# Kernel tuning notes

Hardware: AMD Instinct MI355X
Metric: run time of the kernel (lower is better)

Reference implementation:

```python
import math
import jax, jax.numpy as jnp
import numpy as np

N, T, F, H = 30000, 4, 128, 8  # num_node, num_type, num_fea, num_head
D = F // H


def setup_inputs() -> dict:
    key = jax.random.key(0)
    k0, k1, k2, k3, k4 = jax.random.split(key, 5)
    feature = jax.random.normal(k0, (N, F), dtype=jnp.float32)
    edge_fea = jax.random.normal(k1, (N, T, F), dtype=jnp.float32)
    node_multi_mask = jax.random.randint(k2, (N,), 0, T)
    # Xavier-uniform-like scale for [*, F, F] projection tables
    xav = math.sqrt(6.0 / (F + F))
    node_proj = jax.random.uniform(k3, (T, F, F), minval=-xav, maxval=xav, dtype=jnp.float32)
    edge_proj = jax.random.uniform(k4, (T * T, F, F), minval=-xav, maxval=xav, dtype=jnp.float32)
    return {
        "feature": feature,
        "edge_fea": edge_fea,
        "node_multi_mask": node_multi_mask,
        "node_proj": node_proj,
        "edge_proj": edge_proj,
    }


def reference(feature, edge_fea, node_multi_mask, node_proj, edge_proj):
    # Type-indexed projections. Instead of gathering per-node [F,F] matrices
    # (which would materialize N*F*F), compute projections for all T source
    # types in one batched einsum, then select each node's type with a gather.
    # node: out[n] = node_proj[mask[n]] @ feature[n]
    node_all = jnp.einsum('tgf,nf->ntg', node_proj, feature)           # [N,T,F]
    node_p = jnp.take_along_axis(node_all, node_multi_mask[:, None, None], axis=1)[:, 0]  # [N,F]
    # edge: out[n,j] = edge_proj[mask[n]*T + j] @ edge_fea[n,j]
    edge_proj_r = edge_proj.reshape(T, T, F, F)                         # [src_type, j, F, F]
    edge_all = jnp.einsum('stgf,ntf->nstg', edge_proj_r, edge_fea)      # [N,T_src,T,F]
    edge_p = jnp.take_along_axis(edge_all, node_multi_mask[:, None, None, None], axis=1)[:, 0]  # [N,T,F]

    # multi-head attention weights
    node_multi_in = node_p.reshape(N, 1, H, D).transpose(0, 2, 1, 3) / math.sqrt(D)  # [N,H,1,D]
    edge_multi_in = edge_p.reshape(N, T, H, D).transpose(0, 2, 3, 1)                  # [N,H,D,T]
    scores = jnp.matmul(node_multi_in, edge_multi_in)                                 # [N,H,1,T]
    # NOTE: original uses nn.Softmax(dim=1) -> softmax over the HEAD axis
    all_r_weight = jax.nn.softmax(scores, axis=1).transpose(0, 3, 1, 2)               # [N,T,H,1]
    return all_r_weight
```

## Files before the change

### kernel.cpp

```cpp
#include <hip/hip_runtime.h>
#include <hip/hip_bf16.h>

#define N_NODES 30000
#define T_TYPES 4
#define F_DIM   128
#define H_HEADS 8

typedef __bf16 bf16x8 __attribute__((ext_vector_type(8)));
typedef __bf16 bf16x4 __attribute__((ext_vector_type(4)));
typedef float  floatx4 __attribute__((ext_vector_type(4)));

#define WS_REORDER 64
#define WS_NPB     480256
#define WS_EPB     611328

template <int CTRL>
static __device__ __forceinline__ float dpp_add(float x) {
    int xi = __builtin_bit_cast(int, x);
    int yi = __builtin_amdgcn_update_dpp(xi, xi, CTRL, 0xF, 0xF, true);
    return x + __builtin_bit_cast(float, yi);
}
static __device__ __forceinline__ float sum16(float x) {
    x = dpp_add<0xB1>(x);
    x = dpp_add<0x4E>(x);
    x = dpp_add<0x141>(x);
    x = dpp_add<0x140>(x);
    return x;
}

__global__ __launch_bounds__(256) void prep_bucket_kernel(
    const float* __restrict__ node_proj, const float* __restrict__ edge_proj,
    __bf16* __restrict__ npb, __bf16* __restrict__ epb,
    const int* __restrict__ mask, int* __restrict__ counts, int* __restrict__ reorder)
{
    const int b = blockIdx.x;
    if (b < 320) {
        int i = b * 256 + threadIdx.x;
        int base = i * 4;
        float4 v;
        __bf16* dst;
        if (base < T_TYPES * F_DIM * F_DIM) {
            v = ((const float4*)node_proj)[i];
            dst = npb + base;
        } else {
            int off = base - T_TYPES * F_DIM * F_DIM;
            v = ((const float4*)edge_proj)[off >> 2];
            dst = epb + off;
        }
        bf16x4 w = { (__bf16)v.x, (__bf16)v.y, (__bf16)v.z, (__bf16)v.w };
        *(bf16x4*)dst = w;
    } else {
        int n = (b - 320) * 256 + threadIdx.x;
        int lane = threadIdx.x & 63;
        int t = (n < N_NODES) ? mask[n] : -1;
        #pragma unroll
        for (int tt = 0; tt < T_TYPES; ++tt) {
            unsigned long long bm = __ballot(t == tt);
            if (bm == 0ull) continue;
            int cnt = __popcll(bm);
            int leader = __ffsll((unsigned long long)bm) - 1;
            int base = 0;
            if (lane == leader) base = atomicAdd(&counts[tt], cnt);
            base = __shfl(base, leader);
            if (t == tt) {
                int prefix = __popcll(bm & ((1ull << lane) - 1ull));
                reorder[tt * N_NODES + base + prefix] = n;
            }
        }
    }
}

__global__ __launch_bounds__(512) void main_kernel(
    const float* __restrict__ feature, const float* __restrict__ edge_fea,
    const int* __restrict__ counts, const int* __restrict__ reorder,
    const __bf16* __restrict__ npb, const __bf16* __restrict__ epb,
    float* __restrict__ out)
{
    const int b = blockIdx.x;
    const int t = b & 3;
    const int start = (b >> 2) * 32;
    const int Nt = counts[t];
    if (start >= Nt) return;
    const int valid = min(32, Nt - start);

    __shared__ __bf16 Afeat[32][136];
    __shared__ __bf16 Aedge[4][32][136];
    __shared__ float  sc[32][4][H_HEADS + 1];
    __shared__ int    nidx[32];

    const int tid = threadIdx.x;
    if (tid < 32) {
        int s = (tid < valid) ? tid : (valid - 1);
        nidx[tid] = reorder[t * N_NODES + start + s];
    }
    __syncthreads();

    const int colv = tid & 31;
    const int rowg = tid >> 5;
    #pragma unroll
    for (int it = 0; it < 2; ++it) {
        int row = it * 16 + rowg;
        float4 v = ((const float4*)(feature + (long)nidx[row] * F_DIM))[colv];
        bf16x4 w = { (__bf16)v.x, (__bf16)v.y, (__bf16)v.z, (__bf16)v.w };
        *(bf16x4*)(&Afeat[row][0] + colv * 4) = w;
    }
    #pragma unroll
    for (int it = 0; it < 8; ++it) {
        int row = it * 16 + rowg;
        int j = row >> 5, r = row & 31;
        float4 v = ((const float4*)(edge_fea + ((long)nidx[r] * 4 + j) * F_DIM))[colv];
        bf16x4 w = { (__bf16)v.x, (__bf16)v.y, (__bf16)v.z, (__bf16)v.w };
        *(bf16x4*)(&Aedge[j][r][0] + colv * 4) = w;
    }
    __syncthreads();

    const int lane = tid & 63;
    const int wave = tid >> 6;
    const int ml   = lane & 15;
    const int quad = lane >> 4;
    const int g0   = wave * 16;

    floatx4 accN[2] = {};
    {
        const __bf16* a0 = &Afeat[ml][quad * 8];
        const __bf16* a1 = &Afeat[16 + ml][quad * 8];
        const __bf16* b0 = npb + t * (F_DIM * F_DIM) + (g0 + ml) * F_DIM + quad * 8;
        #pragma unroll
        for (int k0 = 0; k0 < 128; k0 += 32) {
            bf16x8 A0 = *(const bf16x8*)(a0 + k0);
            bf16x8 A1 = *(const bf16x8*)(a1 + k0);
            bf16x8 B0 = *(const bf16x8*)(b0 + k0);
            accN[0] = __builtin_amdgcn_mfma_f32_16x16x32_bf16(A0, B0, accN[0], 0, 0, 0);
            accN[1] = __builtin_amdgcn_mfma_f32_16x16x32_bf16(A1, B0, accN[1], 0, 0, 0);
        }
    }

    #pragma unroll
    for (int j = 0; j < 4; ++j) {
        floatx4 accE[2] = {};
        const __bf16* a0 = &Aedge[j][ml][quad * 8];
        const __bf16* a1 = &Aedge[j][16 + ml][quad * 8];
        const __bf16* b0 = epb + (t * 4 + j) * (F_DIM * F_DIM) + (g0 + ml) * F_DIM + quad * 8;
        #pragma unroll
        for (int k0 = 0; k0 < 128; k0 += 32) {
            bf16x8 A0 = *(const bf16x8*)(a0 + k0);
            bf16x8 A1 = *(const bf16x8*)(a1 + k0);
            bf16x8 B0 = *(const bf16x8*)(b0 + k0);
            accE[0] = __builtin_amdgcn_mfma_f32_16x16x32_bf16(A0, B0, accE[0], 0, 0, 0);
            accE[1] = __builtin_amdgcn_mfma_f32_16x16x32_bf16(A1, B0, accE[1], 0, 0, 0);
        }
        #pragma unroll
        for (int mt = 0; mt < 2; ++mt) {
            floatx4 p = accN[mt] * accE[mt];
            p.x = sum16(p.x);
            p.y = sum16(p.y);
            p.z = sum16(p.z);
            p.w = sum16(p.w);
            if (ml == 0) {
                int mb = mt * 16 + quad * 4;
                sc[mb + 0][j][wave] = p.x * 0.25f;
                sc[mb + 1][j][wave] = p.y * 0.25f;
                sc[mb + 2][j][wave] = p.z * 0.25f;
                sc[mb + 3][j][wave] = p.w * 0.25f;
            }
        }
    }
    __syncthreads();

    if (tid < 128) {
        int node = tid >> 2, j = tid & 3;
        if (node < valid) {
            float v[8], m = -1e30f;
            #pragma unroll
            for (int h = 0; h < 8; ++h) { v[h] = sc[node][j][h]; m = fmaxf(m, v[h]); }
            float s = 0.f;
            #pragma unroll
            for (int h = 0; h < 8; ++h) { v[h] = __expf(v[h] - m); s += v[h]; }
            float r = 1.0f / s;
            float* o = out + (long)nidx[node] * (T_TYPES * H_HEADS) + j * H_HEADS;
            float4 o0 = { v[0] * r, v[1] * r, v[2] * r, v[3] * r };
            float4 o1 = { v[4] * r, v[5] * r, v[6] * r, v[7] * r };
            ((float4*)o)[0] = o0;
            ((float4*)o)[1] = o1;
        }
    }
}

extern "C" void kernel_launch(void* const* d_in, const int* in_sizes, int n_in,
                              void* d_out, int out_size, void* d_ws, size_t ws_size,
                              hipStream_t stream) {
    const float* feature   = (const float*)d_in[0];
    const float* edge_fea  = (const float*)d_in[1];
    const int*   mask      = (const int*)d_in[2];
    const float* node_proj = (const float*)d_in[3];
    const float* edge_proj = (const float*)d_in[4];
    float* out = (float*)d_out;

    char* ws = (char*)d_ws;
    int*    counts  = (int*)ws;
    int*    reorder = (int*)(ws + WS_REORDER);
    __bf16* npb     = (__bf16*)(ws + WS_NPB);
    __bf16* epb     = (__bf16*)(ws + WS_EPB);

    hipMemsetAsync(counts, 0, T_TYPES * sizeof(int), stream);
    int prep_blocks = 320;
    int bucket_blocks = (N_NODES + 255) / 256;
    prep_bucket_kernel<<<prep_blocks + bucket_blocks, 256, 0, stream>>>(
        node_proj, edge_proj, npb, epb, mask, counts, reorder);
    int nblk = ((N_NODES + 31) / 32) * T_TYPES;
    main_kernel<<<nblk, 512, 0, stream>>>(feature, edge_fea, counts, reorder, npb, epb, out);
}
```

Before: 145.2 us.

## Compact block grid by type prefix sums and prefetch projection weights into registers

The main kernel now maps blocks to node types through prefix sums of the per-type counts, so the grid shrinks from four times the node-block count to about one times that, with no early-exit blocks. The node and first edge projection B fragments are loaded from global memory before the barrier, overlapping with the staging of the activation tiles. The next edge type's weights are prefetched during the current type's MFMAs, with a scheduling barrier to keep that order. An occupancy hint is added to the launch bounds. The cost is higher register pressure from holding the prefetched weight fragments.

```diff
diff --git a/kernel.cpp b/kernel.cpp
--- a/kernel.cpp
+++ b/kernel.cpp
@@ -70,17 +70,21 @@
     }
 }
 
-__global__ __launch_bounds__(512) void main_kernel(
+__global__ __launch_bounds__(512, 6) void main_kernel(
     const float* __restrict__ feature, const float* __restrict__ edge_fea,
     const int* __restrict__ counts, const int* __restrict__ reorder,
     const __bf16* __restrict__ npb, const __bf16* __restrict__ epb,
     float* __restrict__ out)
 {
     const int b = blockIdx.x;
-    const int t = b & 3;
-    const int start = (b >> 2) * 32;
-    const int Nt = counts[t];
-    if (start >= Nt) return;
+    const int c0 = counts[0], c1 = counts[1], c2 = counts[2], c3 = counts[3];
+    const int nb0 = (c0 + 31) >> 5, nb1 = (c1 + 31) >> 5, nb2 = (c2 + 31) >> 5, nb3 = (c3 + 31) >> 5;
+    const int p1 = nb0, p2 = p1 + nb1, p3 = p2 + nb2, p4 = p3 + nb3;
+    if (b >= p4) return;
+    const int t = (b >= p1) + (b >= p2) + (b >= p3);
+    const int pb = (t == 0) ? 0 : (t == 1) ? p1 : (t == 2) ? p2 : p3;
+    const int Nt = (t == 0) ? c0 : (t == 1) ? c1 : (t == 2) ? c2 : c3;
+    const int start = (b - pb) * 32;
     const int valid = min(32, Nt - start);
 
     __shared__ __bf16 Afeat[32][136];
@@ -94,6 +98,12 @@
         nidx[tid] = reorder[t * N_NODES + start + s];
     }
     __syncthreads();
+
+    const int lane = tid & 63;
+    const int wave = tid >> 6;
+    const int ml   = lane & 15;
+    const int quad = lane >> 4;
+    const int g0   = wave * 16;
 
     const int colv = tid & 31;
     const int rowg = tid >> 5;
@@ -112,58 +122,98 @@
         bf16x4 w = { (__bf16)v.x, (__bf16)v.y, (__bf16)v.z, (__bf16)v.w };
         *(bf16x4*)(&Aedge[j][r][0] + colv * 4) = w;
     }
+
+    const __bf16* bn  = npb + t * (F_DIM * F_DIM) + (g0 + ml) * F_DIM + quad * 8;
+    const __bf16* be  = epb + (t * 4) * (F_DIM * F_DIM) + (g0 + ml) * F_DIM + quad * 8;
+    bf16x8 Bn0 = *(const bf16x8*)(bn +  0);
+    bf16x8 Bn1 = *(const bf16x8*)(bn + 32);
+    bf16x8 Bn2 = *(const bf16x8*)(bn + 64);
+    bf16x8 Bn3 = *(const bf16x8*)(bn + 96);
+    bf16x8 Bc0 = *(const bf16x8*)(be +  0);
+    bf16x8 Bc1 = *(const bf16x8*)(be + 32);
+    bf16x8 Bc2 = *(const bf16x8*)(be + 64);
+    bf16x8 Bc3 = *(const bf16x8*)(be + 96);
     __syncthreads();
 
-    const int lane = tid & 63;
-    const int wave = tid >> 6;
-    const int ml   = lane & 15;
-    const int quad = lane >> 4;
-    const int g0   = wave * 16;
-
-    floatx4 accN[2] = {};
+    floatx4 accN0 = {0.f, 0.f, 0.f, 0.f};
+    floatx4 accN1 = {0.f, 0.f, 0.f, 0.f};
     {
         const __bf16* a0 = &Afeat[ml][quad * 8];
         const __bf16* a1 = &Afeat[16 + ml][quad * 8];
-        const __bf16* b0 = npb + t * (F_DIM * F_DIM) + (g0 + ml) * F_DIM + quad * 8;
-        #pragma unroll
-        for (int k0 = 0; k0 < 128; k0 += 32) {
-            bf16x8 A0 = *(const bf16x8*)(a0 + k0);
-            bf16x8 A1 = *(const bf16x8*)(a1 + k0);
-            bf16x8 B0 = *(const bf16x8*)(b0 + k0);
-            accN[0] = __builtin_amdgcn_mfma_f32_16x16x32_bf16(A0, B0, accN[0], 0, 0, 0);
-            accN[1] = __builtin_amdgcn_mfma_f32_16x16x32_bf16(A1, B0, accN[1], 0, 0, 0);
-        }
+        bf16x8 A00 = *(const bf16x8*)(a0 +  0);
+        bf16x8 A10 = *(const bf16x8*)(a1 +  0);
+        bf16x8 A01 = *(const bf16x8*)(a0 + 32);
+        bf16x8 A11 = *(const bf16x8*)(a1 + 32);
+        bf16x8 A02 = *(const bf16x8*)(a0 + 64);
+        bf16x8 A12 = *(const bf16x8*)(a1 + 64);
+        bf16x8 A03 = *(const bf16x8*)(a0 + 96);
+        bf16x8 A13 = *(const bf16x8*)(a1 + 96);
+        accN0 = __builtin_amdgcn_mfma_f32_16x16x32_bf16(A00, Bn0, accN0, 0, 0, 0);
+        accN1 = __builtin_amdgcn_mfma_f32_16x16x32_bf16(A10, Bn0, accN1, 0, 0, 0);
+        accN0 = __builtin_amdgcn_mfma_f32_16x16x32_bf16(A01, Bn1, accN0, 0, 0, 0);
+        accN1 = __builtin_amdgcn_mfma_f32_16x16x32_bf16(A11, Bn1, accN1, 0, 0, 0);
+        accN0 = __builtin_amdgcn_mfma_f32_16x16x32_bf16(A02, Bn2, accN0, 0, 0, 0);
+        accN1 = __builtin_amdgcn_mfma_f32_16x16x32_bf16(A12, Bn2, accN1, 0, 0, 0);
+        accN0 = __builtin_amdgcn_mfma_f32_16x16x32_bf16(A03, Bn3, accN0, 0, 0, 0);
+        accN1 = __builtin_amdgcn_mfma_f32_16x16x32_bf16(A13, Bn3, accN1, 0, 0, 0);
     }
 
     #pragma unroll
     for (int j = 0; j < 4; ++j) {
-        floatx4 accE[2] = {};
+        bf16x8 Bf0, Bf1, Bf2, Bf3;
+        if (j < 3) {
+            const __bf16* bf = epb + (t * 4 + j + 1) * (F_DIM * F_DIM) + (g0 + ml) * F_DIM + quad * 8;
+            Bf0 = *(const bf16x8*)(bf +  0);
+            Bf1 = *(const bf16x8*)(bf + 32);
+            Bf2 = *(const bf16x8*)(bf + 64);
+            Bf3 = *(const bf16x8*)(bf + 96);
+        }
+        __builtin_amdgcn_sched_barrier(0);
+
         const __bf16* a0 = &Aedge[j][ml][quad * 8];
         const __bf16* a1 = &Aedge[j][16 + ml][quad * 8];
-        const __bf16* b0 = epb + (t * 4 + j) * (F_DIM * F_DIM) + (g0 + ml) * F_DIM + quad * 8;
-        #pragma unroll
-        for (int k0 = 0; k0 < 128; k0 += 32) {
-            bf16x8 A0 = *(const bf16x8*)(a0 + k0);
-            bf16x8 A1 = *(const bf16x8*)(a1 + k0);
-            bf16x8 B0 = *(const bf16x8*)(b0 + k0);
-            accE[0] = __builtin_amdgcn_mfma_f32_16x16x32_bf16(A0, B0, accE[0], 0, 0, 0);
-            accE[1] = __builtin_amdgcn_mfma_f32_16x16x32_bf16(A1, B0, accE[1], 0, 0, 0);
-        }
-        #pragma unroll
-        for (int mt = 0; mt < 2; ++mt) {
-            floatx4 p = accN[mt] * accE[mt];
-            p.x = sum16(p.x);
-            p.y = sum16(p.y);
-            p.z = sum16(p.z);
-            p.w = sum16(p.w);
+        bf16x8 E00 = *(const bf16x8*)(a0 +  0);
+        bf16x8 E10 = *(const bf16x8*)(a1 +  0);
+        bf16x8 E01 = *(const bf16x8*)(a0 + 32);
+        bf16x8 E11 = *(const bf16x8*)(a1 + 32);
+        bf16x8 E02 = *(const bf16x8*)(a0 + 64);
+        bf16x8 E12 = *(const bf16x8*)(a1 + 64);
+        bf16x8 E03 = *(const bf16x8*)(a0 + 96);
+        bf16x8 E13 = *(const bf16x8*)(a1 + 96);
+        floatx4 accE0 = {0.f, 0.f, 0.f, 0.f};
+        floatx4 accE1 = {0.f, 0.f, 0.f, 0.f};
+        accE0 = __builtin_amdgcn_mfma_f32_16x16x32_bf16(E00, Bc0, accE0, 0, 0, 0);
+        accE1 = __builtin_amdgcn_mfma_f32_16x16x32_bf16(E10, Bc0, accE1, 0, 0, 0);
+        accE0 = __builtin_amdgcn_mfma_f32_16x16x32_bf16(E01, Bc1, accE0, 0, 0, 0);
+        accE1 = __builtin_amdgcn_mfma_f32_16x16x32_bf16(E11, Bc1, accE1, 0, 0, 0);
+        accE0 = __builtin_amdgcn_mfma_f32_16x16x32_bf16(E02, Bc2, accE0, 0, 0, 0);
+        accE1 = __builtin_amdgcn_mfma_f32_16x16x32_bf16(E12, Bc2, accE1, 0, 0, 0);
+        accE0 = __builtin_amdgcn_mfma_f32_16x16x32_bf16(E03, Bc3, accE0, 0, 0, 0);
+        accE1 = __builtin_amdgcn_mfma_f32_16x16x32_bf16(E13, Bc3, accE1, 0, 0, 0);
+
+        {
+            floatx4 p = accN0 * accE0;
+            p.x = sum16(p.x); p.y = sum16(p.y); p.z = sum16(p.z); p.w = sum16(p.w);
             if (ml == 0) {
-                int mb = mt * 16 + quad * 4;
+                int mb = quad * 4;
                 sc[mb + 0][j][wave] = p.x * 0.25f;
                 sc[mb + 1][j][wave] = p.y * 0.25f;
                 sc[mb + 2][j][wave] = p.z * 0.25f;
                 sc[mb + 3][j][wave] = p.w * 0.25f;
             }
         }
+        {
+            floatx4 p = accN1 * accE1;
+            p.x = sum16(p.x); p.y = sum16(p.y); p.z = sum16(p.z); p.w = sum16(p.w);
+            if (ml == 0) {
+                int mb = 16 + quad * 4;
+                sc[mb + 0][j][wave] = p.x * 0.25f;
+                sc[mb + 1][j][wave] = p.y * 0.25f;
+                sc[mb + 2][j][wave] = p.z * 0.25f;
+                sc[mb + 3][j][wave] = p.w * 0.25f;
+            }
+        }
+        if (j < 3) { Bc0 = Bf0; Bc1 = Bf1; Bc2 = Bf2; Bc3 = Bf3; }
     }
     __syncthreads();
 
@@ -207,6 +257,6 @@
     int bucket_blocks = (N_NODES + 255) / 256;
     prep_bucket_kernel<<<prep_blocks + bucket_blocks, 256, 0, stream>>>(
         node_proj, edge_proj, npb, epb, mask, counts, reorder);
-    int nblk = ((N_NODES + 31) / 32) * T_TYPES;
+    int nblk = (N_NODES + 31) / 32 + T_TYPES - 1;
     main_kernel<<<nblk, 512, 0, stream>>>(feature, edge_fea, counts, reorder, npb, epb, out);
 }
```

Result: no change. 144.2 us, median of 2 (-0.6%).

## Compact block mapping over type buckets and halve edge LDS staging

Applied to the files above, without the earlier changes.

Blocks now map densely onto per-type buckets through prefix sums of the counts, so the grid shrinks to about N/32+3 blocks instead of launching four times that and exiting most of them early. The edge-feature LDS buffer is halved by staging two edge types at a time in two phases with an extra barrier. Launch bounds now request higher occupancy. The intent is to cut wasted block launches and LDS pressure so more blocks fit per CU, at the cost of serialising the edge loads into two phases with an extra sync.

```diff
diff --git a/kernel.cpp b/kernel.cpp
--- a/kernel.cpp
+++ b/kernel.cpp
@@ -70,21 +70,25 @@
     }
 }
 
-__global__ __launch_bounds__(512) void main_kernel(
+__global__ __launch_bounds__(512, 8) void main_kernel(
     const float* __restrict__ feature, const float* __restrict__ edge_fea,
     const int* __restrict__ counts, const int* __restrict__ reorder,
     const __bf16* __restrict__ npb, const __bf16* __restrict__ epb,
     float* __restrict__ out)
 {
     const int b = blockIdx.x;
-    const int t = b & 3;
-    const int start = (b >> 2) * 32;
-    const int Nt = counts[t];
-    if (start >= Nt) return;
+    const int c0 = counts[0], c1 = counts[1], c2 = counts[2], c3 = counts[3];
+    const int nb0 = (c0 + 31) >> 5, nb1 = (c1 + 31) >> 5, nb2 = (c2 + 31) >> 5, nb3 = (c3 + 31) >> 5;
+    const int p1 = nb0, p2 = p1 + nb1, p3 = p2 + nb2, p4 = p3 + nb3;
+    if (b >= p4) return;
+    const int t = (b >= p1) + (b >= p2) + (b >= p3);
+    const int pb = (t == 0) ? 0 : (t == 1) ? p1 : (t == 2) ? p2 : p3;
+    const int Nt = (t == 0) ? c0 : (t == 1) ? c1 : (t == 2) ? c2 : c3;
+    const int start = (b - pb) * 32;
     const int valid = min(32, Nt - start);
 
     __shared__ __bf16 Afeat[32][136];
-    __shared__ __bf16 Aedge[4][32][136];
+    __shared__ __bf16 Aedge[2][32][136];
     __shared__ float  sc[32][4][H_HEADS + 1];
     __shared__ int    nidx[32];
 
@@ -105,7 +109,7 @@
         *(bf16x4*)(&Afeat[row][0] + colv * 4) = w;
     }
     #pragma unroll
-    for (int it = 0; it < 8; ++it) {
+    for (int it = 0; it < 4; ++it) {
         int row = it * 16 + rowg;
         int j = row >> 5, r = row & 31;
         float4 v = ((const float4*)(edge_fea + ((long)nidx[r] * 4 + j) * F_DIM))[colv];
@@ -136,7 +140,7 @@
     }
 
     #pragma unroll
-    for (int j = 0; j < 4; ++j) {
+    for (int j = 0; j < 2; ++j) {
         floatx4 accE[2] = {};
         const __bf16* a0 = &Aedge[j][ml][quad * 8];
         const __bf16* a1 = &Aedge[j][16 + ml][quad * 8];
@@ -152,10 +156,46 @@
         #pragma unroll
         for (int mt = 0; mt < 2; ++mt) {
             floatx4 p = accN[mt] * accE[mt];
-            p.x = sum16(p.x);
-            p.y = sum16(p.y);
-            p.z = sum16(p.z);
-            p.w = sum16(p.w);
+            p.x = sum16(p.x); p.y = sum16(p.y); p.z = sum16(p.z); p.w = sum16(p.w);
+            if (ml == 0) {
+                int mb = mt * 16 + quad * 4;
+                sc[mb + 0][j][wave] = p.x * 0.25f;
+                sc[mb + 1][j][wave] = p.y * 0.25f;
+                sc[mb + 2][j][wave] = p.z * 0.25f;
+                sc[mb + 3][j][wave] = p.w * 0.25f;
+            }
+        }
+    }
+    __syncthreads();
+
+    #pragma unroll
+    for (int it = 0; it < 4; ++it) {
+        int row = it * 16 + rowg;
+        int j = row >> 5, r = row & 31;
+        float4 v = ((const float4*)(edge_fea + ((long)nidx[r] * 4 + 2 + j) * F_DIM))[colv];
+        bf16x4 w = { (__bf16)v.x, (__bf16)v.y, (__bf16)v.z, (__bf16)v.w };
+        *(bf16x4*)(&Aedge[j][r][0] + colv * 4) = w;
+    }
+    __syncthreads();
+
+    #pragma unroll
+    for (int j = 2; j < 4; ++j) {
+        floatx4 accE[2] = {};
+        const __bf16* a0 = &Aedge[j - 2][ml][quad * 8];
+        const __bf16* a1 = &Aedge[j - 2][16 + ml][quad * 8];
+        const __bf16* b0 = epb + (t * 4 + j) * (F_DIM * F_DIM) + (g0 + ml) * F_DIM + quad * 8;
+        #pragma unroll
+        for (int k0 = 0; k0 < 128; k0 += 32) {
+            bf16x8 A0 = *(const bf16x8*)(a0 + k0);
+            bf16x8 A1 = *(const bf16x8*)(a1 + k0);
+            bf16x8 B0 = *(const bf16x8*)(b0 + k0);
+            accE[0] = __builtin_amdgcn_mfma_f32_16x16x32_bf16(A0, B0, accE[0], 0, 0, 0);
+            accE[1] = __builtin_amdgcn_mfma_f32_16x16x32_bf16(A1, B0, accE[1], 0, 0, 0);
+        }
+        #pragma unroll
+        for (int mt = 0; mt < 2; ++mt) {
+            floatx4 p = accN[mt] * accE[mt];
+            p.x = sum16(p.x); p.y = sum16(p.y); p.z = sum16(p.z); p.w = sum16(p.w);
             if (ml == 0) {
                 int mb = mt * 16 + quad * 4;
                 sc[mb + 0][j][wave] = p.x * 0.25f;
@@ -207,6 +247,6 @@
     int bucket_blocks = (N_NODES + 255) / 256;
     prep_bucket_kernel<<<prep_blocks + bucket_blocks, 256, 0, stream>>>(
         node_proj, edge_proj, npb, epb, mask, counts, reorder);
-    int nblk = ((N_NODES + 31) / 32) * T_TYPES;
+    int nblk = (N_NODES + 31) / 32 + T_TYPES - 1;
     main_kernel<<<nblk, 512, 0, stream>>>(feature, edge_fea, counts, reorder, npb, epb, out);
 }
```

New measurement: 145.9 us. Within noise of the previous version (+0.5%).
